# Kernel tuning notes

Hardware: AMD Instinct MI355X
Metric: run time of the kernel (lower is better)

The kernel has to match this reference:

```python
import jax, jax.numpy as jnp
import numpy as np

B, J, D, H = 4096, 17, 512, 8
DK = D // H  # 64
NEG = jnp.float32(-9e15)


def _build_adj_mask():
    # Human3.6M 17-joint skeleton (parent indices), symmetric + self-loops,
    # matching SemGCN's adj>0 mask (adj_mx_from_edges adds identity).
    parents = np.array([-1, 0, 1, 2, 0, 4, 5, 0, 7, 8, 9, 8, 11, 12, 8, 14, 15])
    A = np.eye(J, dtype=np.float32)
    for c, p in enumerate(parents):
        if p >= 0:
            A[c, p] = 1.0
            A[p, c] = 1.0
    rows, cols = np.nonzero(A)
    return rows.astype(np.int32), cols.astype(np.int32)


def setup_inputs() -> dict:
    key = jax.random.key(0)
    ks = jax.random.split(key, 16)
    s = 0.02
    rows, cols = _build_adj_mask()
    return {
        "src": jax.random.normal(ks[0], (B, J, D), jnp.float32),
        # per-head Q/K/V Linears, stacked over heads: [H, D, DK]
        "Wq": jax.random.normal(ks[1], (H, D, DK), jnp.float32) * s,
        "bq": jnp.zeros((H, DK), jnp.float32),
        "Wk": jax.random.normal(ks[2], (H, D, DK), jnp.float32) * s,
        "bk": jnp.zeros((H, DK), jnp.float32),
        "Wv": jax.random.normal(ks[3], (H, D, DK), jnp.float32) * s,
        "bv": jnp.zeros((H, DK), jnp.float32),
        # output projection of MultiHeadAttention: [H*DK, D]
        "Wo": jax.random.normal(ks[4], (H * DK, D), jnp.float32) * s,
        "bo": jnp.zeros((D,), jnp.float32),
        "ln1_g": jnp.ones((D,), jnp.float32),
        "ln1_b": jnp.zeros((D,), jnp.float32),
        # SemGraphConv: two weight matrices [2, D, D], edge logits e, bias
        "W_gcn": jax.random.normal(ks[5], (2, D, D), jnp.float32) * s,
        "e_gcn": jax.random.normal(ks[6], (rows.shape[0],), jnp.float32),
        "b_gcn": jnp.zeros((D,), jnp.float32),
        "ln2_g": jnp.ones((D,), jnp.float32),
        "ln2_b": jnp.zeros((D,), jnp.float32),
        "mask_rows": jnp.asarray(rows),
        "mask_cols": jnp.asarray(cols),
    }


def _layernorm(x, g, b, eps=1e-5):
    mu = jnp.mean(x, axis=-1, keepdims=True)
    var = jnp.var(x, axis=-1, keepdims=True)
    return (x - mu) * jax.lax.rsqrt(var + eps) * g + b


def _forward(src, Wq, bq, Wk, bk, Wv, bv, Wo, bo, ln1_g, ln1_b,
             W_gcn, e_gcn, b_gcn, ln2_g, ln2_b, mask_rows, mask_cols):
    # --- multi-head attention (all heads vectorized) ---
    q = jnp.einsum('bjd,hde->bhje', src, Wq) + bq[None, :, None, :]
    k = jnp.einsum('bjd,hde->bhje', src, Wk) + bk[None, :, None, :]
    v = jnp.einsum('bjd,hde->bhje', src, Wv) + bv[None, :, None, :]
    scale = jnp.float32(DK) ** 0.5  # q.size(-1) ** 0.5
    att = jax.nn.softmax(jnp.einsum('bhje,bhke->bhjk', q, k) / scale, axis=-1)
    o = jnp.einsum('bhjk,bhke->bhje', att, v)          # [B,H,J,DK]
    o = o.transpose(0, 2, 1, 3).reshape(B, J, H * DK)  # concat over heads
    attn_out = o @ Wo + bo
    x = _layernorm(src + attn_out, ln1_g, ln1_b)

    # --- SemGraphConv ---
    h0 = x @ W_gcn[0]
    h1 = x @ W_gcn[1]
    logits = jnp.full((J, J), NEG, jnp.float32).at[mask_rows, mask_cols].set(e_gcn)
    A = jax.nn.softmax(logits, axis=1)                 # [J,J]
    I = jnp.eye(J, dtype=jnp.float32)
    gcn = jnp.einsum('jk,bkd->bjd', A * I, h0) + jnp.einsum('jk,bkd->bjd', A * (1.0 - I), h1)
    gcn = gcn + b_gcn
    return _layernorm(x + gcn, ln2_g, ln2_b)


def reference(src, Wq, bq, Wk, bk, Wv, bv, Wo, bo, ln1_g, ln1_b,
              W_gcn, e_gcn, b_gcn, ln2_g, ln2_b, mask_rows, mask_cols):
    return _forward(src, Wq, bq, Wk, bk, Wv, bv, Wo, bo, ln1_g, ln1_b,
                    W_gcn, e_gcn, b_gcn, ln2_g, ln2_b, mask_rows, mask_cols)
```

## Files before the change

kernel.cpp:

```cpp
#include <hip/hip_runtime.h>


typedef __attribute__((ext_vector_type(4))) float floatx4;
typedef __attribute__((ext_vector_type(8))) short short8;

#define AS1 __attribute__((address_space(1)))
#define AS3 __attribute__((address_space(3)))

__device__ __forceinline__ float bf2f(unsigned short u) {
  union { unsigned int i; float f; } x;
  x.i = ((unsigned int)u) << 16;
  return x.f;
}

__device__ __forceinline__ unsigned short f2bf(float f) {
  union { float f; unsigned int i; } x;
  x.f = f;
  unsigned int r = x.i + 0x7fffu + ((x.i >> 16) & 1u);
  return (unsigned short)(r >> 16);
}

__device__ __forceinline__ void unpack8(uint4 u, float* f) {
  unsigned int uu[4] = {u.x, u.y, u.z, u.w};
#pragma unroll
  for (int i = 0; i < 4; ++i) {
    f[2 * i]     = bf2f((unsigned short)(uu[i] & 0xffffu));
    f[2 * i + 1] = bf2f((unsigned short)(uu[i] >> 16));
  }
}

__device__ __forceinline__ uint4 pack8(const float* f) {
  unsigned int uu[4];
#pragma unroll
  for (int i = 0; i < 4; ++i)
    uu[i] = (unsigned int)f2bf(f[2 * i]) | ((unsigned int)f2bf(f[2 * i + 1]) << 16);
  uint4 u; u.x = uu[0]; u.y = uu[1]; u.z = uu[2]; u.w = uu[3];
  return u;
}

__device__ __forceinline__ float wave_sum(float v) {
#pragma unroll
  for (int m = 1; m < 64; m <<= 1) v += __shfl_xor(v, m, 64);
  return v;
}

__device__ __forceinline__ void gload_lds16(const unsigned short* g, AS3 char* l) {
  __builtin_amdgcn_global_load_lds((const AS1 void*)g, (AS3 void*)l, 16, 0, 0);
}

__global__ __launch_bounds__(256) void convert_src(
    const float* __restrict__ in, unsigned short* __restrict__ out) {
  const size_t i = ((size_t)blockIdx.x * 256 + threadIdx.x) * 8;
  const float4 a = *(const float4*)(in + i);
  const float4 b = *(const float4*)(in + i + 4);
  const float f[8] = {a.x, a.y, a.z, a.w, b.x, b.y, b.z, b.w};
  *(uint4*)(out + i) = pack8(f);
}

__global__ __launch_bounds__(256) void gemm_bt(
    const unsigned short* __restrict__ A,
    const unsigned short* __restrict__ BT,
    const float* __restrict__ bias,
    unsigned short* __restrict__ C, int N) {
  __shared__ unsigned short As[3][128 * 32];
  __shared__ unsigned short Bs[3][128 * 32];
  const int t = threadIdx.x;
  const int wave = t >> 6;
  const int lane = t & 63;
  const int wm = wave >> 1, wn = wave & 1;

  const int nTN = N >> 7;
  const int q8 = gridDim.x >> 3;
  const int lin = (blockIdx.x & 7) * q8 + (blockIdx.x >> 3);
  const int tm = lin / nTN;
  const int tn = lin - tm * nTN;
  const long rowBase = (long)tm * 128;
  const long colBase = (long)tn * 128;

  const unsigned short* a0 = A + (size_t)rowBase * 512;
  const unsigned short* b0 = BT + (size_t)colBase * 512;

  floatx4 acc[4][4];
#pragma unroll
  for (int i = 0; i < 4; ++i)
#pragma unroll
    for (int j = 0; j < 4; ++j) acc[i][j] = (floatx4){0.f, 0.f, 0.f, 0.f};

  const int c0 = t, c1 = t + 256;
  const size_t gOff0 =
      (size_t)(c0 >> 2) * 512 + (size_t)((c0 & 3) ^ ((c0 >> 3) & 3)) * 8;
  const size_t gOff1 =
      (size_t)(c1 >> 2) * 512 + (size_t)((c1 & 3) ^ ((c1 >> 3) & 3)) * 8;
  const int ldsByte0 = wave * 1024;
  const int ldsByte1 = 4096 + wave * 1024;

#define STAGE(buf, k0)                                                       \
  do {                                                                       \
    gload_lds16(a0 + gOff0 + (k0), (AS3 char*)&As[(buf)][0] + ldsByte0);     \
    gload_lds16(a0 + gOff1 + (k0), (AS3 char*)&As[(buf)][0] + ldsByte1);     \
    gload_lds16(b0 + gOff0 + (k0), (AS3 char*)&Bs[(buf)][0] + ldsByte0);     \
    gload_lds16(b0 + gOff1 + (k0), (AS3 char*)&Bs[(buf)][0] + ldsByte1);     \
  } while (0)

  const int am = lane & 15;
  const int q = lane >> 4;

  STAGE(0, 0);
  STAGE(1, 32);
  asm volatile("s_waitcnt vmcnt(4)" ::: "memory");
  __builtin_amdgcn_sched_barrier(0);
  __builtin_amdgcn_s_barrier();

#pragma unroll
  for (int kt = 0; kt < 16; ++kt) {
    if (kt + 2 < 16) STAGE((kt + 2) % 3, (kt + 2) * 32);

    const unsigned short* As_ = &As[kt % 3][0];
    const unsigned short* Bs_ = &Bs[kt % 3][0];
    short8 af[4], bf[4];
#pragma unroll
    for (int i = 0; i < 4; ++i) {
      const int row = wm * 64 + i * 16 + am;
      af[i] = *(const short8*)&As_[row * 32 + ((q ^ ((row >> 1) & 3)) << 3)];
    }
#pragma unroll
    for (int j = 0; j < 4; ++j) {
      const int row = wn * 64 + j * 16 + am;
      bf[j] = *(const short8*)&Bs_[row * 32 + ((q ^ ((row >> 1) & 3)) << 3)];
    }
#pragma unroll
    for (int i = 0; i < 4; ++i)
#pragma unroll
      for (int j = 0; j < 4; ++j)
        acc[i][j] = __builtin_amdgcn_mfma_f32_16x16x32_bf16(af[i], bf[j], acc[i][j], 0, 0, 0);

    if (kt == 15) break;
    if (kt < 14) asm volatile("s_waitcnt vmcnt(4)" ::: "memory");
    else         asm volatile("s_waitcnt vmcnt(0)" ::: "memory");
    __builtin_amdgcn_sched_barrier(0);
    __builtin_amdgcn_s_barrier();
  }
#undef STAGE

  const int q4 = (lane >> 4) << 2;
#pragma unroll
  for (int i = 0; i < 4; ++i) {
#pragma unroll
    for (int j = 0; j < 4; ++j) {
      const long col = colBase + wn * 64 + j * 16 + am;
      const float badd = bias ? bias[col] : 0.f;
      const long rowa = rowBase + wm * 64 + i * 16 + q4;
#pragma unroll
      for (int r = 0; r < 4; ++r)
        C[(size_t)(rowa + r) * N + col] = f2bf(acc[i][j][r] + badd);
    }
  }
}

__global__ __launch_bounds__(256) void attn_kernel(
    const unsigned short* __restrict__ qkv, unsigned short* __restrict__ o) {
  __shared__ unsigned short Vl[4][17][76];
  const int t = threadIdx.x;
  const int wave = t >> 6, lane = t & 63;
  const int wid = blockIdx.x * 4 + wave;
  const int b = wid >> 3, h = wid & 7;
  const int e = lane & 15, g = lane >> 4;

  const unsigned short* base = qkv + (size_t)b * 17 * 1536 + h * 64;

  unsigned short (*V)[76] = Vl[wave];
  for (int c = lane; c < 136; c += 64) {
    const int kk = c >> 3, e0 = (c & 7) << 3;
    const uint4 u = *(const uint4*)(base + (size_t)kk * 1536 + 1024 + e0);
    *(uint2*)&V[kk][e0]     = make_uint2(u.x, u.y);
    *(uint2*)&V[kk][e0 + 4] = make_uint2(u.z, u.w);
  }

  const int ko = g << 3;
  const unsigned short* qrow  = base + (size_t)e * 1536;
  const unsigned short* row16 = base + (size_t)16 * 1536;
  const short8 Q0  = *(const short8*)(qrow + ko);
  const short8 Q1  = *(const short8*)(qrow + 32 + ko);
  const short8 K0  = *(const short8*)(qrow + 512 + ko);
  const short8 K1  = *(const short8*)(qrow + 512 + 32 + ko);
  const short8 Qb0 = *(const short8*)(row16 + ko);
  const short8 Qb1 = *(const short8*)(row16 + 32 + ko);
  const short8 Kb0 = *(const short8*)(row16 + 512 + ko);
  const short8 Kb1 = *(const short8*)(row16 + 512 + 32 + ko);

  floatx4 sT[2][2];
#pragma unroll
  for (int i = 0; i < 2; ++i)
#pragma unroll
    for (int j = 0; j < 2; ++j) sT[i][j] = (floatx4){0.f, 0.f, 0.f, 0.f};
  sT[0][0] = __builtin_amdgcn_mfma_f32_16x16x32_bf16(K0, Q0, sT[0][0], 0, 0, 0);
  sT[0][0] = __builtin_amdgcn_mfma_f32_16x16x32_bf16(K1, Q1, sT[0][0], 0, 0, 0);
  sT[0][1] = __builtin_amdgcn_mfma_f32_16x16x32_bf16(K0, Qb0, sT[0][1], 0, 0, 0);
  sT[0][1] = __builtin_amdgcn_mfma_f32_16x16x32_bf16(K1, Qb1, sT[0][1], 0, 0, 0);
  sT[1][0] = __builtin_amdgcn_mfma_f32_16x16x32_bf16(Kb0, Q0, sT[1][0], 0, 0, 0);
  sT[1][0] = __builtin_amdgcn_mfma_f32_16x16x32_bf16(Kb1, Q1, sT[1][0], 0, 0, 0);
  sT[1][1] = __builtin_amdgcn_mfma_f32_16x16x32_bf16(Kb0, Qb0, sT[1][1], 0, 0, 0);
  sT[1][1] = __builtin_amdgcn_mfma_f32_16x16x32_bf16(Kb1, Qb1, sT[1][1], 0, 0, 0);

  short8 PA[2];
#pragma unroll
  for (int ni = 0; ni < 2; ++ni) {
    float v[4];
#pragma unroll
    for (int r = 0; r < 4; ++r) v[r] = sT[0][ni][r] * 0.125f;
    const float v16 = sT[1][ni][0] * 0.125f;
    float m = fmaxf(fmaxf(v[0], v[1]), fmaxf(v[2], v[3]));
    if (g == 0) m = fmaxf(m, v16);
    m = fmaxf(m, __shfl_xor(m, 16, 64));
    m = fmaxf(m, __shfl_xor(m, 32, 64));
    float p[4], sum = 0.f;
#pragma unroll
    for (int r = 0; r < 4; ++r) { p[r] = __expf(v[r] - m); sum += p[r]; }
    float p16 = (g == 0) ? __expf(v16 - m) : 0.f;
    sum += p16;
    sum += __shfl_xor(sum, 16, 64);
    sum += __shfl_xor(sum, 32, 64);
    const float inv = 1.f / sum;
#pragma unroll
    for (int r = 0; r < 4; ++r) p[r] *= inv;
    p16 *= inv;

    const unsigned int lo = (unsigned int)f2bf(p[0]) | ((unsigned int)f2bf(p[1]) << 16);
    const unsigned int hi = (unsigned int)f2bf(p[2]) | ((unsigned int)f2bf(p[3]) << 16);
    const unsigned int w16 = (unsigned int)f2bf(p16);

    const int colsrc = ni ? 0 : e;
    const int s0 = colsrc + ((g & 1) << 5);
    unsigned int w0 = __shfl(lo, s0, 64);
    unsigned int w1 = __shfl(hi, s0, 64);
    unsigned int w2 = __shfl(lo, s0 + 16, 64);
    unsigned int w3 = __shfl(hi, s0 + 16, 64);
    const unsigned int a16 = __shfl(w16, colsrc, 64);
    if (g == 2) { w0 = a16; w1 = 0; w2 = 0; w3 = 0; }
    if (g == 3) { w0 = 0; w1 = 0; w2 = 0; w3 = 0; }
    union { unsigned int u[4]; short8 s; } fa;
    fa.u[0] = w0; fa.u[1] = w1; fa.u[2] = w2; fa.u[3] = w3;
    PA[ni] = fa.s;
  }

  floatx4 o0[4], o1[4];
#pragma unroll
  for (int tt = 0; tt < 4; ++tt) {
    o0[tt] = (floatx4){0.f, 0.f, 0.f, 0.f};
    o1[tt] = (floatx4){0.f, 0.f, 0.f, 0.f};
  }
#pragma unroll
  for (int tt = 0; tt < 4; ++tt) {
    const int c = tt * 16 + e;
    union { unsigned int u[4]; short8 s; } fb;
#pragma unroll
    for (int i = 0; i < 4; ++i) {
      int ka = (g << 3) + 2 * i;
      int kb = ka + 1;
      if (ka > 16) ka = 16;
      if (kb > 16) kb = 16;
      fb.u[i] = (unsigned int)V[ka][c] | ((unsigned int)V[kb][c] << 16);
    }
    o0[tt] = __builtin_amdgcn_mfma_f32_16x16x32_bf16(PA[0], fb.s, o0[tt], 0, 0, 0);
    o1[tt] = __builtin_amdgcn_mfma_f32_16x16x32_bf16(PA[1], fb.s, o1[tt], 0, 0, 0);
  }

  unsigned short* ob = o + (size_t)b * 17 * 512 + h * 64;
#pragma unroll
  for (int tt = 0; tt < 4; ++tt)
#pragma unroll
    for (int r = 0; r < 4; ++r)
      ob[(size_t)(4 * g + r) * 512 + tt * 16 + e] = f2bf(o0[tt][r]);
  if (g == 0) {
#pragma unroll
    for (int tt = 0; tt < 4; ++tt)
      ob[(size_t)16 * 512 + tt * 16 + e] = f2bf(o1[tt][0]);
  }
}

__global__ __launch_bounds__(256) void ln_res_kernel(
    const float* __restrict__ a, const unsigned short* __restrict__ b,
    const float* __restrict__ g, const float* __restrict__ beta,
    unsigned short* __restrict__ out) {
  const long row = (long)blockIdx.x * 4 + (threadIdx.x >> 6);
  const int lane = threadIdx.x & 63;
  const int d0 = lane * 8;

  const float4 a0 = *(const float4*)(a + (size_t)row * 512 + d0);
  const float4 a1 = *(const float4*)(a + (size_t)row * 512 + d0 + 4);
  const float fa[8] = {a0.x, a0.y, a0.z, a0.w, a1.x, a1.y, a1.z, a1.w};
  float fb[8], vals[8];
  unpack8(*(const uint4*)(b + (size_t)row * 512 + d0), fb);
  float s = 0.f, s2 = 0.f;
#pragma unroll
  for (int i = 0; i < 8; ++i) {
    vals[i] = fa[i] + fb[i];
    s += vals[i];
    s2 += vals[i] * vals[i];
  }
  const float mean = wave_sum(s) * (1.f / 512.f);
  const float var = wave_sum(s2) * (1.f / 512.f) - mean * mean;
  const float rs = rsqrtf(var + 1e-5f);

  const float4 g0 = *(const float4*)(g + d0);
  const float4 g1 = *(const float4*)(g + d0 + 4);
  const float4 b0 = *(const float4*)(beta + d0);
  const float4 b1 = *(const float4*)(beta + d0 + 4);
  const float fg[8]  = {g0.x, g0.y, g0.z, g0.w, g1.x, g1.y, g1.z, g1.w};
  const float fbt[8] = {b0.x, b0.y, b0.z, b0.w, b1.x, b1.y, b1.z, b1.w};
  float y[8];
#pragma unroll
  for (int i = 0; i < 8; ++i) y[i] = (vals[i] - mean) * rs * fg[i] + fbt[i];
  *(uint4*)(out + (size_t)row * 512 + d0) = pack8(y);
}

__global__ __launch_bounds__(256) void gcn_ln_kernel(
    const unsigned short* __restrict__ x, const unsigned short* __restrict__ h01,
    const float* __restrict__ Adiag, const int* __restrict__ cnt,
    const int* __restrict__ nbrk, const float* __restrict__ nbrw,
    const float* __restrict__ bgcn,
    const float* __restrict__ g, const float* __restrict__ beta,
    float* __restrict__ out) {
  const long row = (long)blockIdx.x * 4 + (threadIdx.x >> 6);
  const int lane = threadIdx.x & 63;
  const int b = (int)(row / 17);
  const int j = (int)(row - (long)b * 17);
  const int d0 = lane * 8;

  float accv[8];
  {
    const float w = Adiag[j];
    float f[8];
    unpack8(*(const uint4*)(h01 + (size_t)row * 1024 + d0), f);
#pragma unroll
    for (int i = 0; i < 8; ++i) accv[i] = w * f[i];
  }
  const int c = cnt[j];
  for (int nb = 0; nb < c; ++nb) {
    const int kk = nbrk[j * 8 + nb];
    const float w = nbrw[j * 8 + nb];
    float f[8];
    unpack8(*(const uint4*)(h01 + ((size_t)b * 17 + kk) * 1024 + 512 + d0), f);
#pragma unroll
    for (int i = 0; i < 8; ++i) accv[i] += w * f[i];
  }

  float fx[8], vals[8];
  unpack8(*(const uint4*)(x + (size_t)row * 512 + d0), fx);
  const float4 bg0 = *(const float4*)(bgcn + d0);
  const float4 bg1 = *(const float4*)(bgcn + d0 + 4);
  const float fbg[8] = {bg0.x, bg0.y, bg0.z, bg0.w, bg1.x, bg1.y, bg1.z, bg1.w};
  float s = 0.f, s2 = 0.f;
#pragma unroll
  for (int i = 0; i < 8; ++i) {
    vals[i] = fx[i] + accv[i] + fbg[i];
    s += vals[i];
    s2 += vals[i] * vals[i];
  }
  const float mean = wave_sum(s) * (1.f / 512.f);
  const float var = wave_sum(s2) * (1.f / 512.f) - mean * mean;
  const float rs = rsqrtf(var + 1e-5f);

  const float4 g0 = *(const float4*)(g + d0);
  const float4 g1 = *(const float4*)(g + d0 + 4);
  const float4 bb0 = *(const float4*)(beta + d0);
  const float4 bb1 = *(const float4*)(beta + d0 + 4);
  const float fg[8]  = {g0.x, g0.y, g0.z, g0.w, g1.x, g1.y, g1.z, g1.w};
  const float fbt[8] = {bb0.x, bb0.y, bb0.z, bb0.w, bb1.x, bb1.y, bb1.z, bb1.w};
  float4 y0, y1;
  y0.x = (vals[0] - mean) * rs * fg[0] + fbt[0];
  y0.y = (vals[1] - mean) * rs * fg[1] + fbt[1];
  y0.z = (vals[2] - mean) * rs * fg[2] + fbt[2];
  y0.w = (vals[3] - mean) * rs * fg[3] + fbt[3];
  y1.x = (vals[4] - mean) * rs * fg[4] + fbt[4];
  y1.y = (vals[5] - mean) * rs * fg[5] + fbt[5];
  y1.z = (vals[6] - mean) * rs * fg[6] + fbt[6];
  y1.w = (vals[7] - mean) * rs * fg[7] + fbt[7];
  *(float4*)(out + (size_t)row * 512 + d0) = y0;
  *(float4*)(out + (size_t)row * 512 + d0 + 4) = y1;
}

__global__ __launch_bounds__(256) void prep_transpose(
    const float* __restrict__ Wq, const float* __restrict__ Wk,
    const float* __restrict__ Wv, const float* __restrict__ Wo,
    const float* __restrict__ Wg,
    unsigned short* __restrict__ WT1, unsigned short* __restrict__ WT2,
    unsigned short* __restrict__ WT3) {
  const int idx = blockIdx.x * 256 + threadIdx.x;
  if (idx < 786432) {
    const int n = idx >> 9, k = idx & 511;
    const int which = n >> 9, nn = n & 511;
    const int hh = nn >> 6, e = nn & 63;
    const float* W = (which == 0) ? Wq : (which == 1) ? Wk : Wv;
    WT1[idx] = f2bf(W[hh * 32768 + k * 64 + e]);
  } else if (idx < 786432 + 262144) {
    const int i2 = idx - 786432;
    const int n = i2 >> 9, k = i2 & 511;
    WT2[i2] = f2bf(Wo[k * 512 + n]);
  } else {
    const int i3 = idx - 1048576;
    const int n = i3 >> 9, k = i3 & 511;
    const int which = n >> 9, nn = n & 511;
    WT3[i3] = f2bf(Wg[which * 262144 + k * 512 + nn]);
  }
}

__global__ __launch_bounds__(256) void prep_small(
    const float* __restrict__ bq, const float* __restrict__ bk,
    const float* __restrict__ bv, const float* __restrict__ bo,
    const float* __restrict__ e, const int* __restrict__ rows,
    const int* __restrict__ cols, int nnz,
    float* __restrict__ bias1, float* __restrict__ bias2,
    float* __restrict__ Adiag, int* __restrict__ cnt,
    int* __restrict__ nbrk, float* __restrict__ nbrw) {
  const int t = threadIdx.x;
  for (int i = t; i < 1536; i += 256)
    bias1[i] = (i < 512) ? bq[i] : (i < 1024) ? bk[i - 512] : bv[i - 1024];
  for (int i = t; i < 512; i += 256) bias2[i] = bo[i];
  if (t < 17) {
    float m = -1e30f;
    for (int i = 0; i < nnz; ++i)
      if (rows[i] == t) m = fmaxf(m, e[i]);
    float s = 0.f;
    for (int i = 0; i < nnz; ++i)
      if (rows[i] == t) s += __expf(e[i] - m);
    const float inv = 1.f / s;
    int c = 0;
    for (int i = 0; i < nnz; ++i)
      if (rows[i] == t) {
        const float w = __expf(e[i] - m) * inv;
        const int kk = cols[i];
        if (kk == t) Adiag[t] = w;
        else { nbrk[t * 8 + c] = kk; nbrw[t * 8 + c] = w; ++c; }
      }
    cnt[t] = c;
  }
}

extern "C" void kernel_launch(void* const* d_in, const int* in_sizes, int n_in,
                              void* d_out, int out_size, void* d_ws, size_t ws_size,
                              hipStream_t stream) {
  const float* src = (const float*)d_in[0];
  const float* Wq  = (const float*)d_in[1];
  const float* bq  = (const float*)d_in[2];
  const float* Wk  = (const float*)d_in[3];
  const float* bk  = (const float*)d_in[4];
  const float* Wv  = (const float*)d_in[5];
  const float* bv  = (const float*)d_in[6];
  const float* Wo  = (const float*)d_in[7];
  const float* bo  = (const float*)d_in[8];
  const float* ln1g = (const float*)d_in[9];
  const float* ln1b = (const float*)d_in[10];
  const float* Wg  = (const float*)d_in[11];
  const float* eg  = (const float*)d_in[12];
  const float* bg  = (const float*)d_in[13];
  const float* ln2g = (const float*)d_in[14];
  const float* ln2b = (const float*)d_in[15];
  const int* mrows = (const int*)d_in[16];
  const int* mcols = (const int*)d_in[17];
  const int nnz = in_sizes[16];

  float* out = (float*)d_out;
  char* ws = (char*)d_ws;

  unsigned short* WT1 = (unsigned short*)(ws + 0x0000000);
  unsigned short* WT2 = (unsigned short*)(ws + 0x0180000);
  unsigned short* WT3 = (unsigned short*)(ws + 0x0200000);
  float* bias1 = (float*)(ws + 0x0300000);
  float* bias2 = (float*)(ws + 0x0302000);
  float* Adiag = (float*)(ws + 0x0303000);
  int* cnt     = (int*)(ws + 0x0303100);
  int* nbrk    = (int*)(ws + 0x0303200);
  float* nbrw  = (float*)(ws + 0x0303600);
  unsigned short* SRCB = (unsigned short*)(ws + 0x0400000);
  unsigned short* QKV  = (unsigned short*)(ws + 0x4800000);
  unsigned short* O    = (unsigned short*)(ws + 0x0400000);
  unsigned short* ATT  = (unsigned short*)(ws + 0x4800000);
  unsigned short* X    = (unsigned short*)(ws + 0x8C00000);
  unsigned short* H01  = (unsigned short*)(ws + 0x0400000);

  (void)n_in; (void)out_size; (void)ws_size;

  convert_src<<<17408, 256, 0, stream>>>(src, SRCB);
  prep_transpose<<<6144, 256, 0, stream>>>(Wq, Wk, Wv, Wo, Wg, WT1, WT2, WT3);
  prep_small<<<1, 256, 0, stream>>>(bq, bk, bv, bo, eg, mrows, mcols, nnz,
                                    bias1, bias2, Adiag, cnt, nbrk, nbrw);
  gemm_bt<<<6528, 256, 0, stream>>>(SRCB, WT1, bias1, QKV, 1536);
  attn_kernel<<<8192, 256, 0, stream>>>(QKV, O);
  gemm_bt<<<2176, 256, 0, stream>>>(O, WT2, bias2, ATT, 512);
  ln_res_kernel<<<17408, 256, 0, stream>>>(src, ATT, ln1g, ln1b, X);
  gemm_bt<<<4352, 256, 0, stream>>>(X, WT3, nullptr, H01, 1024);
  gcn_ln_kernel<<<17408, 256, 0, stream>>>(X, H01, Adiag, cnt, nbrk, nbrw, bg,
                                           ln2g, ln2b, out);
}
```

Measured before the change: 809.7 us.

## Rewrite bf16 GEMM as 256x256 tile, 8-wave kernel with interleaved LDS prefetch

Replaces the 128x128, 4-wave, triple-buffered GEMM with a 256x256 block tile run by 8 waves, each wave computing 128x64. K is split into 64-wide steps held in a double buffer of two 32-wide halves, 128 KB of LDS in total. Global-to-LDS loads for later steps are placed between MFMA sub-phases, with s_setprio raised around the MFMA bursts to overlap memory and compute. Larger tiles cut global and LDS traffic per flop, at the cost of occupancy from the heavy LDS and register use and of more barriers per step.

```diff
diff --git a/kernel.cpp b/kernel.cpp
--- a/kernel.cpp
+++ b/kernel.cpp
@@ -57,102 +57,173 @@
   *(uint4*)(out + i) = pack8(f);
 }
 
-__global__ __launch_bounds__(256) void gemm_bt(
+__device__ __forceinline__ void stgA(const unsigned short* a0, size_t gTh,
+                                     AS3 char* L, int ldsW, int bb, int kt,
+                                     int kh) {
+  gload_lds16(a0 + gTh + kt * 64 + kh * 32,
+              L + bb * 32768 + kh * 16384 + ldsW);
+  gload_lds16(a0 + gTh + 65536 + kt * 64 + kh * 32,
+              L + bb * 32768 + kh * 16384 + 8192 + ldsW);
+}
+__device__ __forceinline__ void stgB(const unsigned short* b0, size_t gTh,
+                                     AS3 char* L, int ldsW, int bb, int kt,
+                                     int kh) {
+  gload_lds16(b0 + gTh + kt * 64 + kh * 32,
+              L + 65536 + bb * 32768 + kh * 16384 + ldsW);
+  gload_lds16(b0 + gTh + 65536 + kt * 64 + kh * 32,
+              L + 65536 + bb * 32768 + kh * 16384 + 8192 + ldsW);
+}
+
+template <int BB>
+__device__ __forceinline__ void kt_step(
+    int kt, const char* Lr, AS3 char* L,
+    const unsigned short* a0, const unsigned short* b0, size_t gTh, int ldsW,
+    int aBase, int bBase, floatx4 (&acc)[8][4]) {
+  constexpr int base = BB * 32768;
+  short8 afL[4], afH[4], bf[4];
+
+#pragma unroll
+  for (int i = 0; i < 4; ++i)
+    afL[i] = *(const short8*)(Lr + base + aBase + i * 1024);
+#pragma unroll
+  for (int j = 0; j < 4; ++j)
+    bf[j] = *(const short8*)(Lr + base + bBase + j * 1024);
+  if (kt < 7) stgA(a0, gTh, L, ldsW, BB ^ 1, kt + 1, 1);
+  __builtin_amdgcn_s_barrier();
+  asm volatile("s_waitcnt lgkmcnt(0)" ::: "memory");
+  __builtin_amdgcn_sched_barrier(0);
+  __builtin_amdgcn_s_setprio(1);
+#pragma unroll
+  for (int i = 0; i < 4; ++i)
+#pragma unroll
+    for (int j = 0; j < 4; ++j)
+      acc[i][j] = __builtin_amdgcn_mfma_f32_16x16x32_bf16(afL[i], bf[j], acc[i][j], 0, 0, 0);
+  __builtin_amdgcn_s_setprio(0);
+  __builtin_amdgcn_s_barrier();
+
+#pragma unroll
+  for (int i = 0; i < 4; ++i)
+    afH[i] = *(const short8*)(Lr + base + aBase + 4096 + i * 1024);
+  if (kt < 7) stgB(b0, gTh, L, ldsW, BB ^ 1, kt + 1, 1);
+  __builtin_amdgcn_s_barrier();
+  asm volatile("s_waitcnt lgkmcnt(0)" ::: "memory");
+  __builtin_amdgcn_sched_barrier(0);
+  __builtin_amdgcn_s_setprio(1);
+#pragma unroll
+  for (int i = 0; i < 4; ++i)
+#pragma unroll
+    for (int j = 0; j < 4; ++j)
+      acc[4 + i][j] = __builtin_amdgcn_mfma_f32_16x16x32_bf16(afH[i], bf[j], acc[4 + i][j], 0, 0, 0);
+  __builtin_amdgcn_s_setprio(0);
+  if (kt < 7) asm volatile("s_waitcnt vmcnt(8)" ::: "memory");
+  else        asm volatile("s_waitcnt vmcnt(0)" ::: "memory");
+  __builtin_amdgcn_sched_barrier(0);
+  __builtin_amdgcn_s_barrier();
+
+#pragma unroll
+  for (int i = 0; i < 4; ++i)
+    afL[i] = *(const short8*)(Lr + base + 16384 + aBase + i * 1024);
+#pragma unroll
+  for (int j = 0; j < 4; ++j)
+    bf[j] = *(const short8*)(Lr + base + 16384 + bBase + j * 1024);
+  if (kt < 6) stgA(a0, gTh, L, ldsW, BB, kt + 2, 0);
+  __builtin_amdgcn_s_barrier();
+  asm volatile("s_waitcnt lgkmcnt(0)" ::: "memory");
+  __builtin_amdgcn_sched_barrier(0);
+  __builtin_amdgcn_s_setprio(1);
+#pragma unroll
+  for (int i = 0; i < 4; ++i)
+#pragma unroll
+    for (int j = 0; j < 4; ++j)
+      acc[i][j] = __builtin_amdgcn_mfma_f32_16x16x32_bf16(afL[i], bf[j], acc[i][j], 0, 0, 0);
+  __builtin_amdgcn_s_setprio(0);
+  __builtin_amdgcn_s_barrier();
+
+#pragma unroll
+  for (int i = 0; i < 4; ++i)
+    afH[i] = *(const short8*)(Lr + base + 16384 + aBase + 4096 + i * 1024);
+  if (kt < 6) stgB(b0, gTh, L, ldsW, BB, kt + 2, 0);
+  __builtin_amdgcn_s_barrier();
+  asm volatile("s_waitcnt lgkmcnt(0)" ::: "memory");
+  __builtin_amdgcn_sched_barrier(0);
+  __builtin_amdgcn_s_setprio(1);
+#pragma unroll
+  for (int i = 0; i < 4; ++i)
+#pragma unroll
+    for (int j = 0; j < 4; ++j)
+      acc[4 + i][j] = __builtin_amdgcn_mfma_f32_16x16x32_bf16(afH[i], bf[j], acc[4 + i][j], 0, 0, 0);
+  __builtin_amdgcn_s_setprio(0);
+  if (kt < 6)       asm volatile("s_waitcnt vmcnt(8)" ::: "memory");
+  else if (kt == 6) asm volatile("s_waitcnt vmcnt(4)" ::: "memory");
+  __builtin_amdgcn_sched_barrier(0);
+  __builtin_amdgcn_s_barrier();
+}
+
+__global__ __launch_bounds__(512, 2) void gemm_bt(
     const unsigned short* __restrict__ A,
     const unsigned short* __restrict__ BT,
     const float* __restrict__ bias,
     unsigned short* __restrict__ C, int N) {
-  __shared__ unsigned short As[3][128 * 32];
-  __shared__ unsigned short Bs[3][128 * 32];
+  __shared__ char LDSR[131072];
   const int t = threadIdx.x;
-  const int wave = t >> 6;
-  const int lane = t & 63;
-  const int wm = wave >> 1, wn = wave & 1;
-
-  const int nTN = N >> 7;
+  const int wave = t >> 6, lane = t & 63;
+  const int wm = wave >> 2, wn = wave & 3;
+  const int e = lane & 15, g = lane >> 4;
+
+  const int nTN = N >> 8;
   const int q8 = gridDim.x >> 3;
-  const int lin = (blockIdx.x & 7) * q8 + (blockIdx.x >> 3);
+  const int lin = ((int)blockIdx.x & 7) * q8 + ((int)blockIdx.x >> 3);
   const int tm = lin / nTN;
   const int tn = lin - tm * nTN;
-  const long rowBase = (long)tm * 128;
-  const long colBase = (long)tn * 128;
+  const long rowBase = (long)tm * 256;
+  const long colBase = (long)tn * 256;
 
   const unsigned short* a0 = A + (size_t)rowBase * 512;
   const unsigned short* b0 = BT + (size_t)colBase * 512;
 
-  floatx4 acc[4][4];
-#pragma unroll
-  for (int i = 0; i < 4; ++i)
+  const size_t gTh = (size_t)(t >> 2) * 512 +
+                     (size_t)(((t & 3) ^ ((t >> 3) & 3))) * 8;
+  AS3 char* L = (AS3 char*)LDSR;
+  const int ldsW = wave * 1024;
+
+  const int swz16 = ((g ^ ((e >> 1) & 3)) << 4);
+  const char* Lr = LDSR;
+  const int aBase = wm * 8192 + e * 64 + swz16;
+  const int bBase = 65536 + wn * 4096 + e * 64 + swz16;
+
+  floatx4 acc[8][4];
+#pragma unroll
+  for (int i = 0; i < 8; ++i)
 #pragma unroll
     for (int j = 0; j < 4; ++j) acc[i][j] = (floatx4){0.f, 0.f, 0.f, 0.f};
 
-  const int c0 = t, c1 = t + 256;
-  const size_t gOff0 =
-      (size_t)(c0 >> 2) * 512 + (size_t)((c0 & 3) ^ ((c0 >> 3) & 3)) * 8;
-  const size_t gOff1 =
-      (size_t)(c1 >> 2) * 512 + (size_t)((c1 & 3) ^ ((c1 >> 3) & 3)) * 8;
-  const int ldsByte0 = wave * 1024;
-  const int ldsByte1 = 4096 + wave * 1024;
-
-#define STAGE(buf, k0)                                                       \
-  do {                                                                       \
-    gload_lds16(a0 + gOff0 + (k0), (AS3 char*)&As[(buf)][0] + ldsByte0);     \
-    gload_lds16(a0 + gOff1 + (k0), (AS3 char*)&As[(buf)][0] + ldsByte1);     \
-    gload_lds16(b0 + gOff0 + (k0), (AS3 char*)&Bs[(buf)][0] + ldsByte0);     \
-    gload_lds16(b0 + gOff1 + (k0), (AS3 char*)&Bs[(buf)][0] + ldsByte1);     \
-  } while (0)
-
-  const int am = lane & 15;
-  const int q = lane >> 4;
-
-  STAGE(0, 0);
-  STAGE(1, 32);
-  asm volatile("s_waitcnt vmcnt(4)" ::: "memory");
-  __builtin_amdgcn_sched_barrier(0);
-  __builtin_amdgcn_s_barrier();
-
-#pragma unroll
-  for (int kt = 0; kt < 16; ++kt) {
-    if (kt + 2 < 16) STAGE((kt + 2) % 3, (kt + 2) * 32);
-
-    const unsigned short* As_ = &As[kt % 3][0];
-    const unsigned short* Bs_ = &Bs[kt % 3][0];
-    short8 af[4], bf[4];
-#pragma unroll
-    for (int i = 0; i < 4; ++i) {
-      const int row = wm * 64 + i * 16 + am;
-      af[i] = *(const short8*)&As_[row * 32 + ((q ^ ((row >> 1) & 3)) << 3)];
-    }
-#pragma unroll
-    for (int j = 0; j < 4; ++j) {
-      const int row = wn * 64 + j * 16 + am;
-      bf[j] = *(const short8*)&Bs_[row * 32 + ((q ^ ((row >> 1) & 3)) << 3)];
-    }
-#pragma unroll
-    for (int i = 0; i < 4; ++i)
-#pragma unroll
-      for (int j = 0; j < 4; ++j)
-        acc[i][j] = __builtin_amdgcn_mfma_f32_16x16x32_bf16(af[i], bf[j], acc[i][j], 0, 0, 0);
-
-    if (kt == 15) break;
-    if (kt < 14) asm volatile("s_waitcnt vmcnt(4)" ::: "memory");
-    else         asm volatile("s_waitcnt vmcnt(0)" ::: "memory");
-    __builtin_amdgcn_sched_barrier(0);
-    __builtin_amdgcn_s_barrier();
-  }
-#undef STAGE
-
-  const int q4 = (lane >> 4) << 2;
-#pragma unroll
-  for (int i = 0; i < 4; ++i) {
-#pragma unroll
-    for (int j = 0; j < 4; ++j) {
-      const long col = colBase + wn * 64 + j * 16 + am;
+  stgA(a0, gTh, L, ldsW, 0, 0, 0); stgB(b0, gTh, L, ldsW, 0, 0, 0);
+  stgA(a0, gTh, L, ldsW, 0, 0, 1); stgB(b0, gTh, L, ldsW, 0, 0, 1);
+  stgA(a0, gTh, L, ldsW, 1, 1, 0); stgB(b0, gTh, L, ldsW, 1, 1, 0);
+  asm volatile("s_waitcnt vmcnt(8)" ::: "memory");
+  __builtin_amdgcn_sched_barrier(0);
+  __builtin_amdgcn_s_barrier();
+
+#pragma unroll 1
+  for (int ktp = 0; ktp < 4; ++ktp) {
+    kt_step<0>(2 * ktp,     Lr, L, a0, b0, gTh, ldsW, aBase, bBase, acc);
+    kt_step<1>(2 * ktp + 1, Lr, L, a0, b0, gTh, ldsW, aBase, bBase, acc);
+  }
+
+  asm volatile("s_waitcnt vmcnt(0) lgkmcnt(0)" ::: "memory");
+  __builtin_amdgcn_sched_barrier(0);
+
+  const int q4 = g << 2;
+#pragma unroll
+  for (int mf = 0; mf < 8; ++mf) {
+    const long rowa = rowBase + wm * 128 + mf * 16 + q4;
+#pragma unroll
+    for (int nf = 0; nf < 4; ++nf) {
+      const long col = colBase + wn * 64 + nf * 16 + e;
       const float badd = bias ? bias[col] : 0.f;
-      const long rowa = rowBase + wm * 64 + i * 16 + q4;
 #pragma unroll
       for (int r = 0; r < 4; ++r)
-        C[(size_t)(rowa + r) * N + col] = f2bf(acc[i][j][r] + badd);
+        C[(size_t)(rowa + r) * N + col] = f2bf(acc[mf][nf][r] + badd);
     }
   }
 }
@@ -485,11 +556,11 @@
   prep_transpose<<<6144, 256, 0, stream>>>(Wq, Wk, Wv, Wo, Wg, WT1, WT2, WT3);
   prep_small<<<1, 256, 0, stream>>>(bq, bk, bv, bo, eg, mrows, mcols, nnz,
                                     bias1, bias2, Adiag, cnt, nbrk, nbrw);
-  gemm_bt<<<6528, 256, 0, stream>>>(SRCB, WT1, bias1, QKV, 1536);
+  gemm_bt<<<1632, 512, 0, stream>>>(SRCB, WT1, bias1, QKV, 1536);
   attn_kernel<<<8192, 256, 0, stream>>>(QKV, O);
-  gemm_bt<<<2176, 256, 0, stream>>>(O, WT2, bias2, ATT, 512);
+  gemm_bt<<<544, 512, 0, stream>>>(O, WT2, bias2, ATT, 512);
   ln_res_kernel<<<17408, 256, 0, stream>>>(src, ATT, ln1g, ln1b, X);
-  gemm_bt<<<4352, 256, 0, stream>>>(X, WT3, nullptr, H01, 1024);
+  gemm_bt<<<1088, 512, 0, stream>>>(X, WT3, nullptr, H01, 1024);
   gcn_ln_kernel<<<17408, 256, 0, stream>>>(X, H01, Adiag, cnt, nbrk, nbrw, bg,
                                            ln2g, ln2b, out);
 }
```

Result: no change. 795.1 us (-1.8%).
